# Kernel tuning notes

Measured on AMD Instinct MI355X. Metric: run time of the kernel, lower is better.

The kernel has to match this reference:

```python
import jax, jax.numpy as jnp
import numpy as np
from jax import lax

NPOINT, RADIUS, NSAMPLE, EPS = 2048, 0.1, 32, 1e-5


def setup_inputs() -> dict:
    key = jax.random.key(0)
    ks = jax.random.split(key, 8)
    B, N, D, CIN, COUT, DEPTH = 4, 8192, 29, 32, 64, 2
    return {
        "xyz": jax.random.uniform(ks[0], (B, 3, N), jnp.float32),
        "points": jax.random.normal(ks[1], (B, D, N), jnp.float32),
        "proj_w": jax.random.normal(ks[2], (COUT, CIN), jnp.float32) * 0.05,
        "proj_g": jnp.ones((COUT,), jnp.float32),
        "proj_b": jnp.zeros((COUT,), jnp.float32),
        "w1": jax.random.normal(ks[3], (DEPTH, COUT, COUT), jnp.float32) * 0.05,
        "g1": jnp.ones((DEPTH, COUT), jnp.float32),
        "b1": jnp.zeros((DEPTH, COUT), jnp.float32),
        "w2": jax.random.normal(ks[4], (DEPTH, COUT, COUT), jnp.float32) * 0.05,
        "g2": jnp.ones((DEPTH, COUT), jnp.float32),
        "b2": jnp.zeros((DEPTH, COUT), jnp.float32),
    }


def fps(xyz, npoint):
    # xyz: [B,N,3] -> idx [B,npoint]; deterministic start at index 0
    B, N, _ = xyz.shape
    def body(carry, _):
        dist, far = carry  # [B,N], [B]
        centroid = jnp.take_along_axis(xyz, far[:, None, None], axis=1)  # [B,1,3]
        d = jnp.sum((xyz - centroid) ** 2, -1)
        dist = jnp.minimum(dist, d)
        return (dist, jnp.argmax(dist, -1).astype(jnp.int32)), far
    init = (jnp.full((B, N), 1e10, xyz.dtype), jnp.zeros((B,), jnp.int32))
    _, idx = lax.scan(body, init, None, length=npoint)
    return jnp.transpose(idx)  # [B,npoint]


def ball_query(radius, nsample, xyz, new_xyz):
    # matches torch query_ball_point: invalid -> N, sort, take first nsample, backfill
    N = xyz.shape[1]
    sqr = (jnp.sum(new_xyz ** 2, -1)[:, :, None]
           + jnp.sum(xyz ** 2, -1)[:, None, :]
           - 2.0 * jnp.einsum("bsc,bnc->bsn", new_xyz, xyz))  # [B,S,N]
    cand = jnp.where(sqr <= radius * radius, jnp.arange(N, dtype=jnp.int32), jnp.int32(N))
    neg, _ = lax.top_k(-cand, nsample)
    idx = -neg  # nsample smallest indices, ascending
    first = idx[:, :, :1]
    return jnp.where(idx == N, first, idx)  # [B,S,K]


def gather_nb(p, idx):
    # p [B,N,C], idx [B,S,K] -> [B,S,K,C]
    return jax.vmap(lambda pb, ib: pb[ib])(p, idx)


def _conv(x, w):
    # 1x1 conv: w [O,C], x [B,C,K,S]
    return jnp.einsum("oc,bcks->boks", w, x)


def _bn(x, g, b):
    # training-mode BatchNorm2d over (B,K,S) per channel
    m = jnp.mean(x, (0, 2, 3), keepdims=True)
    v = jnp.var(x, (0, 2, 3), keepdims=True)
    return g[None, :, None, None] * (x - m) * lax.rsqrt(v + EPS) + b[None, :, None, None]


def reference(xyz, points, proj_w, proj_g, proj_b, w1, g1, b1, w2, g2, b2):
    xyz_t = jnp.transpose(xyz, (0, 2, 1))      # [B,N,3]
    pts_t = jnp.transpose(points, (0, 2, 1))   # [B,N,D]
    fidx = fps(xyz_t, NPOINT)                  # [B,S]
    new_xyz = jnp.take_along_axis(xyz_t, fidx[:, :, None], axis=1)  # [B,S,3]
    idx = ball_query(RADIUS, NSAMPLE, xyz_t, new_xyz)               # [B,S,K]
    grouped_xyz = gather_nb(xyz_t, idx) - new_xyz[:, :, None, :]    # [B,S,K,3]
    grouped_pts = gather_nb(pts_t, idx)                             # [B,S,K,D]
    new_points = jnp.concatenate([grouped_xyz, grouped_pts], -1)    # [B,S,K,3+D]
    x = jnp.transpose(new_points, (0, 3, 2, 1))                     # [B,C,K,S]
    x = jax.nn.relu(_bn(_conv(x, proj_w), proj_g, proj_b))
    for d in range(w1.shape[0]):
        idn = x
        x = jax.nn.relu(_bn(_conv(x, w1[d]), g1[d], b1[d]))
        x = _bn(_conv(x, w2[d]), g2[d], b2[d])
        x = jax.nn.relu(x + idn)
    feat = jnp.max(x, axis=2)                  # [B,Cout,S]
    return jnp.transpose(new_xyz, (0, 2, 1)), feat
```

## Files before the change

### kernel.cpp

```cpp
#include <hip/hip_runtime.h>
#include <cstdint>
#include <cstddef>

#pragma clang fp contract(off)

#define NPTS    8192
#define NPT     2048
#define KNB     32
#define NB      4
#define DPTS    29
#define CINP    32
#define CO      64
#define KS      (KNB*NPT)
#define TELEM   ((size_t)NB*CO*KS)
#define MCNT    262144.0f
#define BNEPS   1e-5f
#define FTHR    256
#define FWAVES  (FTHR/64)
#define FPT     32

typedef float v2f __attribute__((ext_vector_type(2)));

#define STEP(P, A, B)                                                         \
    {                                                                         \
        v2f dx_ = ax##P + ncx;                                                \
        v2f dy_ = ay##P + ncy;                                                \
        v2f dz_ = az##P + ncz;                                                \
        v2f dd_ = (dx_ * dx_ + dy_ * dy_) + dz_ * dz_;                        \
        float ndA = fminf(d##A, dd_.x);  d##A = ndA;                          \
        float ndB = fminf(d##B, dd_.y);  d##B = ndB;                          \
        tb = fmaxf(tb, fmaxf(ndA, ndB));                                      \
    }

#define SCANK(K) jj = (d##K == tb) ? K : jj;

static __device__ __forceinline__ unsigned long long umax64(unsigned long long a,
                                                            unsigned long long b) {
    return a > b ? a : b;
}

__global__ __launch_bounds__(FTHR, 1) void fps_kernel(const float* __restrict__ xyz,
                                                      float* __restrict__ out0) {
    const int b = blockIdx.x;
    const int t = threadIdx.x;
    const int lane = t & 63;
    const int wid  = t >> 6;
    const float* xb = xyz + (size_t)b * 3 * NPTS;
    const int base = t * FPT;

    extern __shared__ float smem[];
    float* sx = smem;
    float* sy = sx + NPTS;
    float* sz = sy + NPTS;
    float* sc = sz + NPTS;
    unsigned long long* skey = (unsigned long long*)(sc + 3 * NPT);

    v2f ax0,ax1,ax2,ax3,ax4,ax5,ax6,ax7,ax8,ax9,ax10,ax11,ax12,ax13,ax14,ax15;
    v2f ay0,ay1,ay2,ay3,ay4,ay5,ay6,ay7,ay8,ay9,ay10,ay11,ay12,ay13,ay14,ay15;
    v2f az0,az1,az2,az3,az4,az5,az6,az7,az8,az9,az10,az11,az12,az13,az14,az15;
    float d0,d1,d2,d3,d4,d5,d6,d7,d8,d9,d10,d11,d12,d13,d14,d15,
          d16,d17,d18,d19,d20,d21,d22,d23,d24,d25,d26,d27,d28,d29,d30,d31;
    {
        const float4* x4 = (const float4*)(xb + base);
        const float4* y4 = (const float4*)(xb + NPTS + base);
        const float4* z4 = (const float4*)(xb + 2 * NPTS + base);
        float4* lx4 = (float4*)(sx + base);
        float4* ly4 = (float4*)(sy + base);
        float4* lz4 = (float4*)(sz + base);
        float4 v;
        v = x4[0]; lx4[0] = v; ax0  = (v2f){v.x, v.y}; ax1  = (v2f){v.z, v.w};
        v = x4[1]; lx4[1] = v; ax2  = (v2f){v.x, v.y}; ax3  = (v2f){v.z, v.w};
        v = x4[2]; lx4[2] = v; ax4  = (v2f){v.x, v.y}; ax5  = (v2f){v.z, v.w};
        v = x4[3]; lx4[3] = v; ax6  = (v2f){v.x, v.y}; ax7  = (v2f){v.z, v.w};
        v = x4[4]; lx4[4] = v; ax8  = (v2f){v.x, v.y}; ax9  = (v2f){v.z, v.w};
        v = x4[5]; lx4[5] = v; ax10 = (v2f){v.x, v.y}; ax11 = (v2f){v.z, v.w};
        v = x4[6]; lx4[6] = v; ax12 = (v2f){v.x, v.y}; ax13 = (v2f){v.z, v.w};
        v = x4[7]; lx4[7] = v; ax14 = (v2f){v.x, v.y}; ax15 = (v2f){v.z, v.w};
        v = y4[0]; ly4[0] = v; ay0  = (v2f){v.x, v.y}; ay1  = (v2f){v.z, v.w};
        v = y4[1]; ly4[1] = v; ay2  = (v2f){v.x, v.y}; ay3  = (v2f){v.z, v.w};
        v = y4[2]; ly4[2] = v; ay4  = (v2f){v.x, v.y}; ay5  = (v2f){v.z, v.w};
        v = y4[3]; ly4[3] = v; ay6  = (v2f){v.x, v.y}; ay7  = (v2f){v.z, v.w};
        v = y4[4]; ly4[4] = v; ay8  = (v2f){v.x, v.y}; ay9  = (v2f){v.z, v.w};
        v = y4[5]; ly4[5] = v; ay10 = (v2f){v.x, v.y}; ay11 = (v2f){v.z, v.w};
        v = y4[6]; ly4[6] = v; ay12 = (v2f){v.x, v.y}; ay13 = (v2f){v.z, v.w};
        v = y4[7]; ly4[7] = v; ay14 = (v2f){v.x, v.y}; ay15 = (v2f){v.z, v.w};
        v = z4[0]; lz4[0] = v; az0  = (v2f){v.x, v.y}; az1  = (v2f){v.z, v.w};
        v = z4[1]; lz4[1] = v; az2  = (v2f){v.x, v.y}; az3  = (v2f){v.z, v.w};
        v = z4[2]; lz4[2] = v; az4  = (v2f){v.x, v.y}; az5  = (v2f){v.z, v.w};
        v = z4[3]; lz4[3] = v; az6  = (v2f){v.x, v.y}; az7  = (v2f){v.z, v.w};
        v = z4[4]; lz4[4] = v; az8  = (v2f){v.x, v.y}; az9  = (v2f){v.z, v.w};
        v = z4[5]; lz4[5] = v; az10 = (v2f){v.x, v.y}; az11 = (v2f){v.z, v.w};
        v = z4[6]; lz4[6] = v; az12 = (v2f){v.x, v.y}; az13 = (v2f){v.z, v.w};
        v = z4[7]; lz4[7] = v; az14 = (v2f){v.x, v.y}; az15 = (v2f){v.z, v.w};
        d0=d1=d2=d3=d4=d5=d6=d7=d8=d9=d10=d11=d12=d13=d14=d15 = 1e10f;
        d16=d17=d18=d19=d20=d21=d22=d23=d24=d25=d26=d27=d28=d29=d30=d31 = 1e10f;
    }

    float cx = xb[0], cy = xb[NPTS], cz = xb[2 * NPTS];
    float* ob = out0 + (size_t)b * 3 * NPT;
    if (t == 0) { sc[0] = cx; sc[NPT] = cy; sc[2 * NPT] = cz; }

    for (int i = 1; i < NPT; ++i) {
        const v2f ncx = (v2f){-cx, -cx};
        const v2f ncy = (v2f){-cy, -cy};
        const v2f ncz = (v2f){-cz, -cz};
        float tb = -1.0f;
        STEP(0, 0, 1)    STEP(1, 2, 3)    STEP(2, 4, 5)    STEP(3, 6, 7)
        STEP(4, 8, 9)    STEP(5, 10, 11)  STEP(6, 12, 13)  STEP(7, 14, 15)
        STEP(8, 16, 17)  STEP(9, 18, 19)  STEP(10, 20, 21) STEP(11, 22, 23)
        STEP(12, 24, 25) STEP(13, 26, 27) STEP(14, 28, 29) STEP(15, 30, 31)

        int jj = 0;
        SCANK(31) SCANK(30) SCANK(29) SCANK(28) SCANK(27) SCANK(26)
        SCANK(25) SCANK(24) SCANK(23) SCANK(22) SCANK(21) SCANK(20)
        SCANK(19) SCANK(18) SCANK(17) SCANK(16) SCANK(15) SCANK(14)
        SCANK(13) SCANK(12) SCANK(11) SCANK(10) SCANK(9)  SCANK(8)
        SCANK(7)  SCANK(6)  SCANK(5)  SCANK(4)  SCANK(3)  SCANK(2)
        SCANK(1)  SCANK(0)
        const int gidx = base + jj;

        float r = tb;
        asm volatile(
            "s_nop 1\n\t"
            "v_max_f32 %0, %0, %0 row_shr:1\n\t"
            "s_nop 1\n\t"
            "v_max_f32 %0, %0, %0 row_shr:2\n\t"
            "s_nop 1\n\t"
            "v_max_f32 %0, %0, %0 row_shr:4\n\t"
            "s_nop 1\n\t"
            "v_max_f32 %0, %0, %0 row_shr:8\n\t"
            "s_nop 1\n\t"
            "v_max_f32 %0, %0, %0 row_bcast:15 row_mask:0xa\n\t"
            "s_nop 1\n\t"
            "v_max_f32 %0, %0, %0 row_bcast:31 row_mask:0xc\n\t"
            "s_nop 1"
            : "+v"(r));
        const float wm = __uint_as_float(
            (unsigned int)__builtin_amdgcn_readlane((int)__float_as_uint(r), 63));

        unsigned long long eq = __ballot(tb == wm);
        const int lwin = __ffsll((long long)eq) - 1;
        const int wgid = __builtin_amdgcn_readlane(gidx, lwin);

        const int par = i & 1;
        if (lane == 0)
            skey[par * FWAVES + wid] =
                (((unsigned long long)__float_as_uint(wm)) << 32) |
                (unsigned int)(~(unsigned int)wgid);
        __syncthreads();

        const ulonglong2* sk2 = (const ulonglong2*)(skey + par * FWAVES);
        ulonglong2 k01 = sk2[0], k23 = sk2[1];
        unsigned long long kbest = umax64(umax64(k01.x, k01.y),
                                          umax64(k23.x, k23.y));
        const int widx = (int)(~(unsigned int)kbest);

        cx = sx[widx]; cy = sy[widx]; cz = sz[widx];
        if (t == 0) { sc[i] = cx; sc[NPT + i] = cy; sc[2 * NPT + i] = cz; }
    }

    __syncthreads();
    const float4* s4 = (const float4*)sc;
    float4* o4 = (float4*)ob;
#pragma unroll
    for (int e = t; e < 3 * NPT / 4; e += FTHR) o4[e] = s4[e];
}

__global__ __launch_bounds__(256) void ballq_kernel(const float* __restrict__ xyz,
                                                    const float* __restrict__ out0,
                                                    int* __restrict__ idx) {
    const int gw   = (blockIdx.x * 256 + threadIdx.x) >> 6;
    const int lane = threadIdx.x & 63;
    const int b  = gw >> 11;
    const int si = gw & 2047;
    const float* xb = xyz + (size_t)b * 3 * NPTS;

    const float cx = out0[b * 3 * NPT + si];
    const float cy = out0[b * 3 * NPT + NPT + si];
    const float cz = out0[b * 3 * NPT + 2*NPT + si];
    const float csum = __fadd_rn(__fadd_rn(__fmul_rn(cx, cx), __fmul_rn(cy, cy)),
                                 __fmul_rn(cz, cz));
    const float R2 = (float)(0.1 * 0.1);

    __shared__ int buf[4][KNB];
    int* mybuf = buf[threadIdx.x >> 6];

    int cnt = 0;
    for (int n0 = 0; n0 < NPTS && cnt < KNB; n0 += 64) {
        const int i = n0 + lane;
        float pxv = xb[i], pyv = xb[NPTS + i], pzv = xb[2 * NPTS + i];
        float ps = __fadd_rn(__fadd_rn(__fmul_rn(pxv, pxv), __fmul_rn(pyv, pyv)),
                             __fmul_rn(pzv, pzv));
        float dot = __fmaf_rn(pzv, cz, __fmaf_rn(pyv, cy, __fmul_rn(pxv, cx)));
        float sqr = __fsub_rn(__fadd_rn(csum, ps), __fadd_rn(dot, dot));
        bool hit = (sqr <= R2);
        unsigned long long m = __ballot(hit);
        int pos = cnt + __popcll(m & ((1ull << lane) - 1ull));
        if (hit && pos < KNB) mybuf[pos] = i;
        cnt += __popcll(m);
    }
    int c = cnt < KNB ? cnt : KNB;
    int first = (cnt > 0) ? mybuf[0] : 0;
    if (lane < KNB) {
        int v = (lane < c) ? mybuf[lane] : first;
        idx[((size_t)gw << 5) + lane] = v;
    }
}

__global__ __launch_bounds__(256) void proj_kernel(const float* __restrict__ xyz,
                                                   const float* __restrict__ points,
                                                   const float* __restrict__ out0,
                                                   const int* __restrict__ idx,
                                                   const float* __restrict__ W,
                                                   float* __restrict__ out,
                                                   float* __restrict__ stats) {
    const int p = blockIdx.x * 256 + threadIdx.x;
    const int b = p >> 16;
    const int q = p & 65535;
    const int k = q >> 11;
    const int s = q & 2047;
    const int tid = threadIdx.x;

    __shared__ float ssum[CO], ssq[CO];
    if (tid < CO) { ssum[tid] = 0.f; ssq[tid] = 0.f; }
    __syncthreads();

    const int j = idx[((size_t)(b * NPT + s) << 5) + k];
    const float* xb = xyz + (size_t)b * 3 * NPTS;
    float a[CINP];
    a[0] = xb[j]            - out0[b * 3 * NPT + s];
    a[1] = xb[NPTS + j]     - out0[b * 3 * NPT + NPT + s];
    a[2] = xb[2*NPTS + j]   - out0[b * 3 * NPT + 2*NPT + s];
    const float* pb = points + (size_t)b * DPTS * NPTS;
#pragma unroll
    for (int c = 0; c < DPTS; ++c) a[3 + c] = pb[c * NPTS + j];

    const size_t obase = (size_t)b * CO * KS + q;
    for (int o = 0; o < CO; ++o) {
        float acc = 0.f;
#pragma unroll
        for (int c = 0; c < CINP; ++c) acc = __fmaf_rn(W[o * CINP + c], a[c], acc);
        out[obase + (size_t)o * KS] = acc;
        float s1 = acc, s2 = acc * acc;
#pragma unroll
        for (int off = 32; off > 0; off >>= 1) {
            s1 += __shfl_xor(s1, off, 64);
            s2 += __shfl_xor(s2, off, 64);
        }
        if ((tid & 63) == 0) { atomicAdd(&ssum[o], s1); atomicAdd(&ssq[o], s2); }
    }
    __syncthreads();
    if (tid < CO) {
        atomicAdd(&stats[tid], ssum[tid]);
        atomicAdd(&stats[CO + tid], ssq[tid]);
    }
}

template <bool HAS_IDN, bool WRITE_ACT>
__global__ __launch_bounds__(256) void conv_bn_kernel(const float* in,
                                                      const float* idn,
                                                      const float* __restrict__ stats_in,
                                                      const float* __restrict__ gamma,
                                                      const float* __restrict__ beta,
                                                      const float* __restrict__ W,
                                                      float* act_out,
                                                      float* out,
                                                      float* __restrict__ stats_out) {
    const int p = blockIdx.x * 256 + threadIdx.x;
    const int b = p >> 16;
    const int q = p & 65535;
    const int tid = threadIdx.x;

    __shared__ float ssc[CO], ssh[CO], ssum[CO], ssq[CO];
    if (tid < CO) {
        const float Minv = 1.0f / MCNT;
        float m = stats_in[tid] * Minv;
        float v = stats_in[CO + tid] * Minv - m * m;
        float scl = gamma[tid] * rsqrtf(v + BNEPS);
        ssc[tid] = scl;
        ssh[tid] = beta[tid] - m * scl;
        ssum[tid] = 0.f; ssq[tid] = 0.f;
    }
    __syncthreads();

    const size_t base = (size_t)b * CO * KS + q;
    float a[CO];
#pragma unroll
    for (int c = 0; c < CO; ++c) {
        float v = __fmaf_rn(ssc[c], in[base + (size_t)c * KS], ssh[c]);
        if (HAS_IDN) v += idn[base + (size_t)c * KS];
        v = fmaxf(v, 0.0f);
        a[c] = v;
        if (WRITE_ACT) act_out[base + (size_t)c * KS] = v;
    }
    for (int o = 0; o < CO; ++o) {
        float acc = 0.f;
#pragma unroll
        for (int c = 0; c < CO; ++c) acc = __fmaf_rn(W[o * CO + c], a[c], acc);
        out[base + (size_t)o * KS] = acc;
        float s1 = acc, s2 = acc * acc;
#pragma unroll
        for (int off = 32; off > 0; off >>= 1) {
            s1 += __shfl_xor(s1, off, 64);
            s2 += __shfl_xor(s2, off, 64);
        }
        if ((tid & 63) == 0) { atomicAdd(&ssum[o], s1); atomicAdd(&ssq[o], s2); }
    }
    __syncthreads();
    if (tid < CO) {
        atomicAdd(&stats_out[tid], ssum[tid]);
        atomicAdd(&stats_out[CO + tid], ssq[tid]);
    }
}

__global__ __launch_bounds__(256) void final_kernel(const float* __restrict__ y2,
                                                    const float* __restrict__ idn,
                                                    const float* __restrict__ stats,
                                                    const float* __restrict__ gamma,
                                                    const float* __restrict__ beta,
                                                    float* __restrict__ feat) {
    const int p = blockIdx.x * 256 + threadIdx.x;
    const int s = p & 2047;
    const int o = (p >> 11) & 63;
    const int b = p >> 17;
    const float Minv = 1.0f / MCNT;
    float m = stats[o] * Minv;
    float v = stats[CO + o] * Minv - m * m;
    float scl = gamma[o] * rsqrtf(v + BNEPS);
    float sh  = beta[o] - m * scl;
    const size_t base = (size_t)b * CO * KS + (size_t)o * KS + s;
    float mx = -1e30f;
#pragma unroll
    for (int k = 0; k < KNB; ++k) {
        float val = __fmaf_rn(scl, y2[base + (size_t)k * NPT], sh) + idn[base + (size_t)k * NPT];
        val = fmaxf(val, 0.0f);
        mx = fmaxf(mx, val);
    }
    feat[p] = mx;
}

__global__ void zero_kernel(float* p, int n) {
    int i = blockIdx.x * blockDim.x + threadIdx.x;
    if (i < n) p[i] = 0.f;
}

extern "C" void kernel_launch(void* const* d_in, const int* in_sizes, int n_in,
                              void* d_out, int out_size, void* d_ws, size_t ws_size,
                              hipStream_t stream) {
    (void)in_sizes; (void)n_in; (void)out_size; (void)ws_size;
    const float* xyz    = (const float*)d_in[0];
    const float* points = (const float*)d_in[1];
    const float* proj_w = (const float*)d_in[2];
    const float* proj_g = (const float*)d_in[3];
    const float* proj_b = (const float*)d_in[4];
    const float* w1     = (const float*)d_in[5];
    const float* g1     = (const float*)d_in[6];
    const float* b1     = (const float*)d_in[7];
    const float* w2     = (const float*)d_in[8];
    const float* g2     = (const float*)d_in[9];
    const float* b2     = (const float*)d_in[10];

    float* out0 = (float*)d_out;
    float* feat = (float*)d_out + NB * 3 * NPT;

    float* stats = (float*)d_ws;
    int*   idx   = (int*)((float*)d_ws + 1024);
    float* A     = (float*)(idx + NB * NPT * KNB);
    float* B     = A + TELEM;

    const size_t fps_lds = (size_t)(3 * NPTS + 3 * NPT) * sizeof(float)
                         + 2 * FWAVES * sizeof(unsigned long long);

    hipLaunchKernelGGL(zero_kernel, dim3(3), dim3(256), 0, stream, stats, 5 * 2 * CO);
    hipLaunchKernelGGL(fps_kernel, dim3(NB), dim3(FTHR), fps_lds, stream, xyz, out0);
    hipLaunchKernelGGL(ballq_kernel, dim3(2048), dim3(256), 0, stream, xyz, out0, idx);
    hipLaunchKernelGGL(proj_kernel, dim3(1024), dim3(256), 0, stream,
                       xyz, points, out0, idx, proj_w, A, stats);
    hipLaunchKernelGGL((conv_bn_kernel<false, true>), dim3(1024), dim3(256), 0, stream,
                       A, (const float*)nullptr, stats, proj_g, proj_b, w1,
                       B, A, stats + 128);
    hipLaunchKernelGGL((conv_bn_kernel<false, false>), dim3(1024), dim3(256), 0, stream,
                       A, (const float*)nullptr, stats + 128, g1, b1, w2,
                       (float*)nullptr, A, stats + 256);
    hipLaunchKernelGGL((conv_bn_kernel<true, true>), dim3(1024), dim3(256), 0, stream,
                       A, B, stats + 256, g2, b2, w1 + CO * CO,
                       B, A, stats + 384);
    hipLaunchKernelGGL((conv_bn_kernel<false, false>), dim3(1024), dim3(256), 0, stream,
                       A, (const float*)nullptr, stats + 384, g1 + CO, b1 + CO, w2 + CO * CO,
                       (float*)nullptr, A, stats + 512);
    hipLaunchKernelGGL(final_kernel, dim3(2048), dim3(256), 0, stream,
                       A, B, stats + 512, g2 + CO, b2 + CO, feat);
}
```

Measured before the change: 2.347 ms.

## Fuse FPS, ball query and projection into a persistent producer-consumer kernel

Merges the FPS, ball-query and projection kernels into one persistent launch. The first four blocks run FPS and publish progress counters every 64 centroids, while the remaining blocks pull work items from an atomic queue, spin-wait on that progress, then run the ball query and the projection conv for two centroids per wave. The aim is to hide the serial FPS latency behind the downstream work and to drop the idx round trip through global memory. The risks are that correctness depends on all blocks being co-resident, that the polling adds overhead, and that the projection stats now go straight to global atomics instead of being reduced in LDS first.

After: 2.795 ms. 19.0% more time.

```diff
diff --git a/kernel.cpp b/kernel.cpp
--- a/kernel.cpp
+++ b/kernel.cpp
@@ -18,6 +18,7 @@
 #define FTHR    256
 #define FWAVES  (FTHR/64)
 #define FPT     32
+#define NTASK   (NB*NPT)
 
 typedef float v2f __attribute__((ext_vector_type(2)));
 
@@ -39,220 +40,246 @@
     return a > b ? a : b;
 }
 
-__global__ __launch_bounds__(FTHR, 1) void fps_kernel(const float* __restrict__ xyz,
-                                                      float* __restrict__ out0) {
-    const int b = blockIdx.x;
+__global__ __launch_bounds__(FTHR, 1) void front_kernel(const float* __restrict__ xyz,
+                                                        const float* __restrict__ points,
+                                                        const float* __restrict__ proj_w,
+                                                        float* __restrict__ out0,
+                                                        float* __restrict__ A,
+                                                        float* stats) {
     const int t = threadIdx.x;
     const int lane = t & 63;
     const int wid  = t >> 6;
-    const float* xb = xyz + (size_t)b * 3 * NPTS;
-    const int base = t * FPT;
 
     extern __shared__ float smem[];
-    float* sx = smem;
-    float* sy = sx + NPTS;
-    float* sz = sy + NPTS;
-    float* sc = sz + NPTS;
-    unsigned long long* skey = (unsigned long long*)(sc + 3 * NPT);
-
-    v2f ax0,ax1,ax2,ax3,ax4,ax5,ax6,ax7,ax8,ax9,ax10,ax11,ax12,ax13,ax14,ax15;
-    v2f ay0,ay1,ay2,ay3,ay4,ay5,ay6,ay7,ay8,ay9,ay10,ay11,ay12,ay13,ay14,ay15;
-    v2f az0,az1,az2,az3,az4,az5,az6,az7,az8,az9,az10,az11,az12,az13,az14,az15;
-    float d0,d1,d2,d3,d4,d5,d6,d7,d8,d9,d10,d11,d12,d13,d14,d15,
-          d16,d17,d18,d19,d20,d21,d22,d23,d24,d25,d26,d27,d28,d29,d30,d31;
+    __shared__ int sidx[FWAVES][2][KNB];
+
+    unsigned* prog = (unsigned*)(stats + 640);
+    unsigned* ctr  = (unsigned*)(stats + 644);
+
+    if (blockIdx.x < NB) {
+        const int b = blockIdx.x;
+        const float* xb = xyz + (size_t)b * 3 * NPTS;
+        const int base = t * FPT;
+
+        float* sx = smem;
+        float* sy = sx + NPTS;
+        float* sz = sy + NPTS;
+        float* sc = sz + NPTS;
+        unsigned long long* skey = (unsigned long long*)(sc + 3 * NPT);
+
+        v2f ax0,ax1,ax2,ax3,ax4,ax5,ax6,ax7,ax8,ax9,ax10,ax11,ax12,ax13,ax14,ax15;
+        v2f ay0,ay1,ay2,ay3,ay4,ay5,ay6,ay7,ay8,ay9,ay10,ay11,ay12,ay13,ay14,ay15;
+        v2f az0,az1,az2,az3,az4,az5,az6,az7,az8,az9,az10,az11,az12,az13,az14,az15;
+        float d0,d1,d2,d3,d4,d5,d6,d7,d8,d9,d10,d11,d12,d13,d14,d15,
+              d16,d17,d18,d19,d20,d21,d22,d23,d24,d25,d26,d27,d28,d29,d30,d31;
+        {
+            const float4* x4 = (const float4*)(xb + base);
+            const float4* y4 = (const float4*)(xb + NPTS + base);
+            const float4* z4 = (const float4*)(xb + 2 * NPTS + base);
+            float4* lx4 = (float4*)(sx + base);
+            float4* ly4 = (float4*)(sy + base);
+            float4* lz4 = (float4*)(sz + base);
+            float4 v;
+            v = x4[0]; lx4[0] = v; ax0  = (v2f){v.x, v.y}; ax1  = (v2f){v.z, v.w};
+            v = x4[1]; lx4[1] = v; ax2  = (v2f){v.x, v.y}; ax3  = (v2f){v.z, v.w};
+            v = x4[2]; lx4[2] = v; ax4  = (v2f){v.x, v.y}; ax5  = (v2f){v.z, v.w};
+            v = x4[3]; lx4[3] = v; ax6  = (v2f){v.x, v.y}; ax7  = (v2f){v.z, v.w};
+            v = x4[4]; lx4[4] = v; ax8  = (v2f){v.x, v.y}; ax9  = (v2f){v.z, v.w};
+            v = x4[5]; lx4[5] = v; ax10 = (v2f){v.x, v.y}; ax11 = (v2f){v.z, v.w};
+            v = x4[6]; lx4[6] = v; ax12 = (v2f){v.x, v.y}; ax13 = (v2f){v.z, v.w};
+            v = x4[7]; lx4[7] = v; ax14 = (v2f){v.x, v.y}; ax15 = (v2f){v.z, v.w};
+            v = y4[0]; ly4[0] = v; ay0  = (v2f){v.x, v.y}; ay1  = (v2f){v.z, v.w};
+            v = y4[1]; ly4[1] = v; ay2  = (v2f){v.x, v.y}; ay3  = (v2f){v.z, v.w};
+            v = y4[2]; ly4[2] = v; ay4  = (v2f){v.x, v.y}; ay5  = (v2f){v.z, v.w};
+            v = y4[3]; ly4[3] = v; ay6  = (v2f){v.x, v.y}; ay7  = (v2f){v.z, v.w};
+            v = y4[4]; ly4[4] = v; ay8  = (v2f){v.x, v.y}; ay9  = (v2f){v.z, v.w};
+            v = y4[5]; ly4[5] = v; ay10 = (v2f){v.x, v.y}; ay11 = (v2f){v.z, v.w};
+            v = y4[6]; ly4[6] = v; ay12 = (v2f){v.x, v.y}; ay13 = (v2f){v.z, v.w};
+            v = y4[7]; ly4[7] = v; ay14 = (v2f){v.x, v.y}; ay15 = (v2f){v.z, v.w};
+            v = z4[0]; lz4[0] = v; az0  = (v2f){v.x, v.y}; az1  = (v2f){v.z, v.w};
+            v = z4[1]; lz4[1] = v; az2  = (v2f){v.x, v.y}; az3  = (v2f){v.z, v.w};
+            v = z4[2]; lz4[2] = v; az4  = (v2f){v.x, v.y}; az5  = (v2f){v.z, v.w};
+            v = z4[3]; lz4[3] = v; az6  = (v2f){v.x, v.y}; az7  = (v2f){v.z, v.w};
+            v = z4[4]; lz4[4] = v; az8  = (v2f){v.x, v.y}; az9  = (v2f){v.z, v.w};
+            v = z4[5]; lz4[5] = v; az10 = (v2f){v.x, v.y}; az11 = (v2f){v.z, v.w};
+            v = z4[6]; lz4[6] = v; az12 = (v2f){v.x, v.y}; az13 = (v2f){v.z, v.w};
+            v = z4[7]; lz4[7] = v; az14 = (v2f){v.x, v.y}; az15 = (v2f){v.z, v.w};
+            d0=d1=d2=d3=d4=d5=d6=d7=d8=d9=d10=d11=d12=d13=d14=d15 = 1e10f;
+            d16=d17=d18=d19=d20=d21=d22=d23=d24=d25=d26=d27=d28=d29=d30=d31 = 1e10f;
+        }
+
+        float cx = xb[0], cy = xb[NPTS], cz = xb[2 * NPTS];
+        float* ob = out0 + (size_t)b * 3 * NPT;
+        if (t == 0) { sc[0] = cx; sc[NPT] = cy; sc[2 * NPT] = cz; }
+
+        for (int i = 1; i < NPT; ++i) {
+            const v2f ncx = (v2f){-cx, -cx};
+            const v2f ncy = (v2f){-cy, -cy};
+            const v2f ncz = (v2f){-cz, -cz};
+            float tb = -1.0f;
+            STEP(0, 0, 1)    STEP(1, 2, 3)    STEP(2, 4, 5)    STEP(3, 6, 7)
+            STEP(4, 8, 9)    STEP(5, 10, 11)  STEP(6, 12, 13)  STEP(7, 14, 15)
+            STEP(8, 16, 17)  STEP(9, 18, 19)  STEP(10, 20, 21) STEP(11, 22, 23)
+            STEP(12, 24, 25) STEP(13, 26, 27) STEP(14, 28, 29) STEP(15, 30, 31)
+
+            int jj = 0;
+            SCANK(31) SCANK(30) SCANK(29) SCANK(28) SCANK(27) SCANK(26)
+            SCANK(25) SCANK(24) SCANK(23) SCANK(22) SCANK(21) SCANK(20)
+            SCANK(19) SCANK(18) SCANK(17) SCANK(16) SCANK(15) SCANK(14)
+            SCANK(13) SCANK(12) SCANK(11) SCANK(10) SCANK(9)  SCANK(8)
+            SCANK(7)  SCANK(6)  SCANK(5)  SCANK(4)  SCANK(3)  SCANK(2)
+            SCANK(1)  SCANK(0)
+            const int gidx = base + jj;
+
+            float r = tb;
+            asm volatile(
+                "s_nop 1\n\t"
+                "v_max_f32 %0, %0, %0 row_shr:1\n\t"
+                "s_nop 1\n\t"
+                "v_max_f32 %0, %0, %0 row_shr:2\n\t"
+                "s_nop 1\n\t"
+                "v_max_f32 %0, %0, %0 row_shr:4\n\t"
+                "s_nop 1\n\t"
+                "v_max_f32 %0, %0, %0 row_shr:8\n\t"
+                "s_nop 1\n\t"
+                "v_max_f32 %0, %0, %0 row_bcast:15 row_mask:0xa\n\t"
+                "s_nop 1\n\t"
+                "v_max_f32 %0, %0, %0 row_bcast:31 row_mask:0xc\n\t"
+                "s_nop 1"
+                : "+v"(r));
+            const float wm = __uint_as_float(
+                (unsigned int)__builtin_amdgcn_readlane((int)__float_as_uint(r), 63));
+
+            unsigned long long eq = __ballot(tb == wm);
+            const int lwin = __ffsll((long long)eq) - 1;
+            const int wgid = __builtin_amdgcn_readlane(gidx, lwin);
+
+            const int par = i & 1;
+            if (lane == 0)
+                skey[par * FWAVES + wid] =
+                    (((unsigned long long)__float_as_uint(wm)) << 32) |
+                    (unsigned int)(~(unsigned int)wgid);
+            __syncthreads();
+
+            const ulonglong2* sk2 = (const ulonglong2*)(skey + par * FWAVES);
+            ulonglong2 k01 = sk2[0], k23 = sk2[1];
+            unsigned long long kbest = umax64(umax64(k01.x, k01.y),
+                                              umax64(k23.x, k23.y));
+            const int widx = (int)(~(unsigned int)kbest);
+
+            cx = sx[widx]; cy = sy[widx]; cz = sz[widx];
+            if (t == 0) {
+                sc[i] = cx; sc[NPT + i] = cy; sc[2 * NPT + i] = cz;
+                if ((i & 63) == 63) {
+                    const int i0 = i - 63;
+                    const float4* p4x = (const float4*)(sc + i0);
+                    const float4* p4y = (const float4*)(sc + NPT + i0);
+                    const float4* p4z = (const float4*)(sc + 2 * NPT + i0);
+                    float4* o4x = (float4*)(ob + i0);
+                    float4* o4y = (float4*)(ob + NPT + i0);
+                    float4* o4z = (float4*)(ob + 2 * NPT + i0);
+#pragma unroll
+                    for (int u = 0; u < 16; ++u) {
+                        o4x[u] = p4x[u]; o4y[u] = p4y[u]; o4z[u] = p4z[u];
+                    }
+                    __threadfence();
+                    atomicExch(&prog[b], (unsigned)(i + 1));
+                }
+            }
+        }
+        return;
+    }
+
     {
-        const float4* x4 = (const float4*)(xb + base);
-        const float4* y4 = (const float4*)(xb + NPTS + base);
-        const float4* z4 = (const float4*)(xb + 2 * NPTS + base);
-        float4* lx4 = (float4*)(sx + base);
-        float4* ly4 = (float4*)(sy + base);
-        float4* lz4 = (float4*)(sz + base);
-        float4 v;
-        v = x4[0]; lx4[0] = v; ax0  = (v2f){v.x, v.y}; ax1  = (v2f){v.z, v.w};
-        v = x4[1]; lx4[1] = v; ax2  = (v2f){v.x, v.y}; ax3  = (v2f){v.z, v.w};
-        v = x4[2]; lx4[2] = v; ax4  = (v2f){v.x, v.y}; ax5  = (v2f){v.z, v.w};
-        v = x4[3]; lx4[3] = v; ax6  = (v2f){v.x, v.y}; ax7  = (v2f){v.z, v.w};
-        v = x4[4]; lx4[4] = v; ax8  = (v2f){v.x, v.y}; ax9  = (v2f){v.z, v.w};
-        v = x4[5]; lx4[5] = v; ax10 = (v2f){v.x, v.y}; ax11 = (v2f){v.z, v.w};
-        v = x4[6]; lx4[6] = v; ax12 = (v2f){v.x, v.y}; ax13 = (v2f){v.z, v.w};
-        v = x4[7]; lx4[7] = v; ax14 = (v2f){v.x, v.y}; ax15 = (v2f){v.z, v.w};
-        v = y4[0]; ly4[0] = v; ay0  = (v2f){v.x, v.y}; ay1  = (v2f){v.z, v.w};
-        v = y4[1]; ly4[1] = v; ay2  = (v2f){v.x, v.y}; ay3  = (v2f){v.z, v.w};
-        v = y4[2]; ly4[2] = v; ay4  = (v2f){v.x, v.y}; ay5  = (v2f){v.z, v.w};
-        v = y4[3]; ly4[3] = v; ay6  = (v2f){v.x, v.y}; ay7  = (v2f){v.z, v.w};
-        v = y4[4]; ly4[4] = v; ay8  = (v2f){v.x, v.y}; ay9  = (v2f){v.z, v.w};
-        v = y4[5]; ly4[5] = v; ay10 = (v2f){v.x, v.y}; ay11 = (v2f){v.z, v.w};
-        v = y4[6]; ly4[6] = v; ay12 = (v2f){v.x, v.y}; ay13 = (v2f){v.z, v.w};
-        v = y4[7]; ly4[7] = v; ay14 = (v2f){v.x, v.y}; ay15 = (v2f){v.z, v.w};
-        v = z4[0]; lz4[0] = v; az0  = (v2f){v.x, v.y}; az1  = (v2f){v.z, v.w};
-        v = z4[1]; lz4[1] = v; az2  = (v2f){v.x, v.y}; az3  = (v2f){v.z, v.w};
-        v = z4[2]; lz4[2] = v; az4  = (v2f){v.x, v.y}; az5  = (v2f){v.z, v.w};
-        v = z4[3]; lz4[3] = v; az6  = (v2f){v.x, v.y}; az7  = (v2f){v.z, v.w};
-        v = z4[4]; lz4[4] = v; az8  = (v2f){v.x, v.y}; az9  = (v2f){v.z, v.w};
-        v = z4[5]; lz4[5] = v; az10 = (v2f){v.x, v.y}; az11 = (v2f){v.z, v.w};
-        v = z4[6]; lz4[6] = v; az12 = (v2f){v.x, v.y}; az13 = (v2f){v.z, v.w};
-        v = z4[7]; lz4[7] = v; az14 = (v2f){v.x, v.y}; az15 = (v2f){v.z, v.w};
-        d0=d1=d2=d3=d4=d5=d6=d7=d8=d9=d10=d11=d12=d13=d14=d15 = 1e10f;
-        d16=d17=d18=d19=d20=d21=d22=d23=d24=d25=d26=d27=d28=d29=d30=d31 = 1e10f;
-    }
-
-    float cx = xb[0], cy = xb[NPTS], cz = xb[2 * NPTS];
-    float* ob = out0 + (size_t)b * 3 * NPT;
-    if (t == 0) { sc[0] = cx; sc[NPT] = cy; sc[2 * NPT] = cz; }
-
-    for (int i = 1; i < NPT; ++i) {
-        const v2f ncx = (v2f){-cx, -cx};
-        const v2f ncy = (v2f){-cy, -cy};
-        const v2f ncz = (v2f){-cz, -cz};
-        float tb = -1.0f;
-        STEP(0, 0, 1)    STEP(1, 2, 3)    STEP(2, 4, 5)    STEP(3, 6, 7)
-        STEP(4, 8, 9)    STEP(5, 10, 11)  STEP(6, 12, 13)  STEP(7, 14, 15)
-        STEP(8, 16, 17)  STEP(9, 18, 19)  STEP(10, 20, 21) STEP(11, 22, 23)
-        STEP(12, 24, 25) STEP(13, 26, 27) STEP(14, 28, 29) STEP(15, 30, 31)
-
-        int jj = 0;
-        SCANK(31) SCANK(30) SCANK(29) SCANK(28) SCANK(27) SCANK(26)
-        SCANK(25) SCANK(24) SCANK(23) SCANK(22) SCANK(21) SCANK(20)
-        SCANK(19) SCANK(18) SCANK(17) SCANK(16) SCANK(15) SCANK(14)
-        SCANK(13) SCANK(12) SCANK(11) SCANK(10) SCANK(9)  SCANK(8)
-        SCANK(7)  SCANK(6)  SCANK(5)  SCANK(4)  SCANK(3)  SCANK(2)
-        SCANK(1)  SCANK(0)
-        const int gidx = base + jj;
-
-        float r = tb;
-        asm volatile(
-            "s_nop 1\n\t"
-            "v_max_f32 %0, %0, %0 row_shr:1\n\t"
-            "s_nop 1\n\t"
-            "v_max_f32 %0, %0, %0 row_shr:2\n\t"
-            "s_nop 1\n\t"
-            "v_max_f32 %0, %0, %0 row_shr:4\n\t"
-            "s_nop 1\n\t"
-            "v_max_f32 %0, %0, %0 row_shr:8\n\t"
-            "s_nop 1\n\t"
-            "v_max_f32 %0, %0, %0 row_bcast:15 row_mask:0xa\n\t"
-            "s_nop 1\n\t"
-            "v_max_f32 %0, %0, %0 row_bcast:31 row_mask:0xc\n\t"
-            "s_nop 1"
-            : "+v"(r));
-        const float wm = __uint_as_float(
-            (unsigned int)__builtin_amdgcn_readlane((int)__float_as_uint(r), 63));
-
-        unsigned long long eq = __ballot(tb == wm);
-        const int lwin = __ffsll((long long)eq) - 1;
-        const int wgid = __builtin_amdgcn_readlane(gidx, lwin);
-
-        const int par = i & 1;
-        if (lane == 0)
-            skey[par * FWAVES + wid] =
-                (((unsigned long long)__float_as_uint(wm)) << 32) |
-                (unsigned int)(~(unsigned int)wgid);
-        __syncthreads();
-
-        const ulonglong2* sk2 = (const ulonglong2*)(skey + par * FWAVES);
-        ulonglong2 k01 = sk2[0], k23 = sk2[1];
-        unsigned long long kbest = umax64(umax64(k01.x, k01.y),
-                                          umax64(k23.x, k23.y));
-        const int widx = (int)(~(unsigned int)kbest);
-
-        cx = sx[widx]; cy = sy[widx]; cz = sz[widx];
-        if (t == 0) { sc[i] = cx; sc[NPT + i] = cy; sc[2 * NPT + i] = cz; }
-    }
-
-    __syncthreads();
-    const float4* s4 = (const float4*)sc;
-    float4* o4 = (float4*)ob;
-#pragma unroll
-    for (int e = t; e < 3 * NPT / 4; e += FTHR) o4[e] = s4[e];
-}
-
-__global__ __launch_bounds__(256) void ballq_kernel(const float* __restrict__ xyz,
-                                                    const float* __restrict__ out0,
-                                                    int* __restrict__ idx) {
-    const int gw   = (blockIdx.x * 256 + threadIdx.x) >> 6;
-    const int lane = threadIdx.x & 63;
-    const int b  = gw >> 11;
-    const int si = gw & 2047;
-    const float* xb = xyz + (size_t)b * 3 * NPTS;
-
-    const float cx = out0[b * 3 * NPT + si];
-    const float cy = out0[b * 3 * NPT + NPT + si];
-    const float cz = out0[b * 3 * NPT + 2*NPT + si];
-    const float csum = __fadd_rn(__fadd_rn(__fmul_rn(cx, cx), __fmul_rn(cy, cy)),
-                                 __fmul_rn(cz, cz));
-    const float R2 = (float)(0.1 * 0.1);
-
-    __shared__ int buf[4][KNB];
-    int* mybuf = buf[threadIdx.x >> 6];
-
-    int cnt = 0;
-    for (int n0 = 0; n0 < NPTS && cnt < KNB; n0 += 64) {
-        const int i = n0 + lane;
-        float pxv = xb[i], pyv = xb[NPTS + i], pzv = xb[2 * NPTS + i];
-        float ps = __fadd_rn(__fadd_rn(__fmul_rn(pxv, pxv), __fmul_rn(pyv, pyv)),
-                             __fmul_rn(pzv, pzv));
-        float dot = __fmaf_rn(pzv, cz, __fmaf_rn(pyv, cy, __fmul_rn(pxv, cx)));
-        float sqr = __fsub_rn(__fadd_rn(csum, ps), __fadd_rn(dot, dot));
-        bool hit = (sqr <= R2);
-        unsigned long long m = __ballot(hit);
-        int pos = cnt + __popcll(m & ((1ull << lane) - 1ull));
-        if (hit && pos < KNB) mybuf[pos] = i;
-        cnt += __popcll(m);
-    }
-    int c = cnt < KNB ? cnt : KNB;
-    int first = (cnt > 0) ? mybuf[0] : 0;
-    if (lane < KNB) {
-        int v = (lane < c) ? mybuf[lane] : first;
-        idx[((size_t)gw << 5) + lane] = v;
-    }
-}
-
-__global__ __launch_bounds__(256) void proj_kernel(const float* __restrict__ xyz,
-                                                   const float* __restrict__ points,
-                                                   const float* __restrict__ out0,
-                                                   const int* __restrict__ idx,
-                                                   const float* __restrict__ W,
-                                                   float* __restrict__ out,
-                                                   float* __restrict__ stats) {
-    const int p = blockIdx.x * 256 + threadIdx.x;
-    const int b = p >> 16;
-    const int q = p & 65535;
-    const int k = q >> 11;
-    const int s = q & 2047;
-    const int tid = threadIdx.x;
-
-    __shared__ float ssum[CO], ssq[CO];
-    if (tid < CO) { ssum[tid] = 0.f; ssq[tid] = 0.f; }
-    __syncthreads();
-
-    const int j = idx[((size_t)(b * NPT + s) << 5) + k];
-    const float* xb = xyz + (size_t)b * 3 * NPTS;
-    float a[CINP];
-    a[0] = xb[j]            - out0[b * 3 * NPT + s];
-    a[1] = xb[NPTS + j]     - out0[b * 3 * NPT + NPT + s];
-    a[2] = xb[2*NPTS + j]   - out0[b * 3 * NPT + 2*NPT + s];
-    const float* pb = points + (size_t)b * DPTS * NPTS;
-#pragma unroll
-    for (int c = 0; c < DPTS; ++c) a[3 + c] = pb[c * NPTS + j];
-
-    const size_t obase = (size_t)b * CO * KS + q;
-    for (int o = 0; o < CO; ++o) {
-        float acc = 0.f;
-#pragma unroll
-        for (int c = 0; c < CINP; ++c) acc = __fmaf_rn(W[o * CINP + c], a[c], acc);
-        out[obase + (size_t)o * KS] = acc;
-        float s1 = acc, s2 = acc * acc;
-#pragma unroll
-        for (int off = 32; off > 0; off >>= 1) {
-            s1 += __shfl_xor(s1, off, 64);
-            s2 += __shfl_xor(s2, off, 64);
+        const float R2 = (float)(0.1 * 0.1);
+        int* mybuf0 = &sidx[wid][0][0];
+        int* mybuf1 = &sidx[wid][1][0];
+
+        for (;;) {
+            unsigned tau0 = 0;
+            if (lane == 0) tau0 = atomicAdd(ctr, 2u);
+            tau0 = (unsigned)__builtin_amdgcn_readfirstlane((int)tau0);
+            if (tau0 >= (unsigned)NTASK) break;
+
+            int cnt2[2];
+#pragma unroll
+            for (int h = 0; h < 2; ++h) {
+                const unsigned tau = tau0 + (unsigned)h;
+                const int b  = (int)(tau >> 11);
+                const int si = (int)(tau & 2047);
+                unsigned pv;
+                do {
+                    pv = 0;
+                    if (lane == 0) pv = atomicOr(&prog[b], 0u);
+                    pv = (unsigned)__builtin_amdgcn_readfirstlane((int)pv);
+                    if (pv <= (unsigned)si) __builtin_amdgcn_s_sleep(127);
+                } while (pv <= (unsigned)si);
+                __threadfence();
+
+                const float* xb = xyz + (size_t)b * 3 * NPTS;
+                const float cx = out0[b * 3 * NPT + si];
+                const float cy = out0[b * 3 * NPT + NPT + si];
+                const float cz = out0[b * 3 * NPT + 2 * NPT + si];
+                const float csum = __fadd_rn(__fadd_rn(__fmul_rn(cx, cx),
+                                                       __fmul_rn(cy, cy)),
+                                             __fmul_rn(cz, cz));
+                int* mybuf = h ? mybuf1 : mybuf0;
+                int cnt = 0;
+                for (int n0 = 0; n0 < NPTS && cnt < KNB; n0 += 64) {
+                    const int i = n0 + lane;
+                    float pxv = xb[i], pyv = xb[NPTS + i], pzv = xb[2 * NPTS + i];
+                    float ps = __fadd_rn(__fadd_rn(__fmul_rn(pxv, pxv),
+                                                   __fmul_rn(pyv, pyv)),
+                                         __fmul_rn(pzv, pzv));
+                    float dot = __fmaf_rn(pzv, cz, __fmaf_rn(pyv, cy, __fmul_rn(pxv, cx)));
+                    float sqr = __fsub_rn(__fadd_rn(csum, ps), __fadd_rn(dot, dot));
+                    bool hit = (sqr <= R2);
+                    unsigned long long m = __ballot(hit);
+                    int pos = cnt + __popcll(m & ((1ull << lane) - 1ull));
+                    if (hit && pos < KNB) mybuf[pos] = i;
+                    cnt += __popcll(m);
+                }
+                cnt2[h] = cnt;
+            }
+
+            {
+                const int h = lane >> 5;
+                const int k = lane & 31;
+                const unsigned tau = tau0 + (unsigned)h;
+                const int b = (int)(tau >> 11);
+                const int s = (int)(tau & 2047);
+                const int cnt = h ? cnt2[1] : cnt2[0];
+                const int* mybuf = h ? mybuf1 : mybuf0;
+                const int c = cnt < KNB ? cnt : KNB;
+                const int first = (cnt > 0) ? mybuf[0] : 0;
+                const int j = (k < c) ? mybuf[k] : first;
+
+                const float* xb = xyz + (size_t)b * 3 * NPTS;
+                float a[CINP];
+                a[0] = xb[j]            - out0[b * 3 * NPT + s];
+                a[1] = xb[NPTS + j]     - out0[b * 3 * NPT + NPT + s];
+                a[2] = xb[2 * NPTS + j] - out0[b * 3 * NPT + 2 * NPT + s];
+                const float* pb = points + (size_t)b * DPTS * NPTS;
+#pragma unroll
+                for (int cc = 0; cc < DPTS; ++cc) a[3 + cc] = pb[cc * NPTS + j];
+
+                const size_t obase = (size_t)b * CO * KS + (size_t)k * NPT + s;
+                for (int o = 0; o < CO; ++o) {
+                    float acc = 0.f;
+#pragma unroll
+                    for (int cc = 0; cc < CINP; ++cc)
+                        acc = __fmaf_rn(proj_w[o * CINP + cc], a[cc], acc);
+                    A[obase + (size_t)o * KS] = acc;
+                    float s1 = acc, s2 = acc * acc;
+#pragma unroll
+                    for (int off = 32; off > 0; off >>= 1) {
+                        s1 += __shfl_xor(s1, off, 64);
+                        s2 += __shfl_xor(s2, off, 64);
+                    }
+                    if (lane == 0) { atomicAdd(&stats[o], s1); atomicAdd(&stats[CO + o], s2); }
+                }
+            }
         }
-        if ((tid & 63) == 0) { atomicAdd(&ssum[o], s1); atomicAdd(&ssq[o], s2); }
-    }
-    __syncthreads();
-    if (tid < CO) {
-        atomicAdd(&stats[tid], ssum[tid]);
-        atomicAdd(&stats[CO + tid], ssq[tid]);
     }
 }
 
@@ -371,11 +398,9 @@
     const size_t fps_lds = (size_t)(3 * NPTS + 3 * NPT) * sizeof(float)
                          + 2 * FWAVES * sizeof(unsigned long long);
 
-    hipLaunchKernelGGL(zero_kernel, dim3(3), dim3(256), 0, stream, stats, 5 * 2 * CO);
-    hipLaunchKernelGGL(fps_kernel, dim3(NB), dim3(FTHR), fps_lds, stream, xyz, out0);
-    hipLaunchKernelGGL(ballq_kernel, dim3(2048), dim3(256), 0, stream, xyz, out0, idx);
-    hipLaunchKernelGGL(proj_kernel, dim3(1024), dim3(256), 0, stream,
-                       xyz, points, out0, idx, proj_w, A, stats);
+    hipLaunchKernelGGL(zero_kernel, dim3(3), dim3(256), 0, stream, stats, 656);
+    hipLaunchKernelGGL(front_kernel, dim3(256), dim3(FTHR), fps_lds, stream,
+                       xyz, points, proj_w, out0, A, stats);
     hipLaunchKernelGGL((conv_bn_kernel<false, true>), dim3(1024), dim3(256), 0, stream,
                        A, (const float*)nullptr, stats, proj_g, proj_b, w1,
                        B, A, stats + 128);
```
